# Optimization experiments

Hardware: AMD Instinct MI355X
Metric: run time of the kernel (lower is better)

Reference implementation:

```python
import jax, jax.numpy as jnp
import numpy as np
from jax import lax

B_SZ, D_SPEC, P, NC, MLP_D = 4096, 30, 9, 64, 64
L = P * P + 1  # 82 tokens (81 spiral + cls)


def _spiral_idx(patch=P):
    # Replicates Scan.forward's hardcoded assignments_map: center pixel, then
    # concentric rings (top row, right col, bottom row, left col), each of length 2r.
    cen = patch // 2
    rows, cols = [cen], [cen]
    for r in range(1, cen + 1):
        rows += [cen - r] * (2 * r); cols += list(range(cen - r + 1, cen + r + 1))
        rows += list(range(cen - r + 1, cen + r + 1)); cols += [cen + r] * (2 * r)
        rows += [cen + r] * (2 * r); cols += list(range(cen - r, cen + r))
        rows += list(range(cen - r, cen + r)); cols += [cen - r] * (2 * r)
    return np.asarray(rows), np.asarray(cols)

_ROWS, _COLS = _spiral_idx()


def _ln(x, g, b, eps=1e-5):
    m = x.mean(-1, keepdims=True)
    v = ((x - m) ** 2).mean(-1, keepdims=True)
    return (x - m) * lax.rsqrt(v + eps) * g + b


def _bn(x, g, b, m, v, nspatial, eps=1e-5):
    sh = (1, -1) + (1,) * nspatial
    return (x - m.reshape(sh)) * lax.rsqrt(v.reshape(sh) + eps) * g.reshape(sh) + b.reshape(sh)


def setup_inputs():
    key = jax.random.key(0)
    ks = iter(jax.random.split(key, 40))
    def rn(shape, s=0.1):
        return s * jax.random.normal(next(ks), shape, jnp.float32)
    return {
        "input_data": jax.random.normal(next(ks), (B_SZ, 1, D_SPEC, P, P), jnp.float32),
        "w3": rn((8, 1, 3, 3, 3)), "b3": rn((8,)),
        "g3": 1.0 + rn((8,)), "be3": rn((8,)), "m3": jnp.zeros((8,)), "v3": jnp.ones((8,)),
        "w2c": rn((NC, 8 * D_SPEC, 3, 3)), "b2c": rn((NC,)),
        "g2": 1.0 + rn((NC,)), "be2": rn((NC,)), "m2": jnp.zeros((NC,)), "v2": jnp.ones((NC,)),
        "pos_emb": rn((1, L, NC)), "cls_tok": rn((1, 1, NC)),
        "ln1_g": jnp.ones((NC,)), "ln1_b": jnp.zeros((NC,)),
        "Wb": rn((NC, NC)), "bb": rn((NC,)),
        "Wc": rn((NC, NC)), "bc": rn((NC,)),
        "Wd": rn((NC, NC)), "bd": rn((NC,)),
        "delta_p": rn((1, L, NC)), "A_p": rn((L, NC)),
        "Wst": rn((NC, NC)), "bst": rn((NC,)), "bias_st": rn((1, 1, NC)),
        "ln2_g": jnp.ones((NC,)), "ln2_b": jnp.zeros((NC,)),
        "Wm1": rn((NC, MLP_D)), "bm1": rn((MLP_D,)),
        "Wm2": rn((MLP_D, NC)), "bm2": rn((NC,)),
    }


def _forward(input_data, w3, b3, g3, be3, m3, v3, w2c, b2c, g2, be2, m2, v2,
             pos_emb, cls_tok, ln1_g, ln1_b, Wb, bb, Wc, bc, Wd, bd,
             delta_p, A_p, Wst, bst, bias_st, ln2_g, ln2_b, Wm1, bm1, Wm2, bm2):
    b = input_data.shape[0]
    # conv3d (SAME, k=3) + BN(eval) + ReLU
    h = lax.conv_general_dilated(input_data, w3, (1, 1, 1), [(1, 1)] * 3,
                                 dimension_numbers=("NCDHW", "OIDHW", "NCDHW"))
    h = jax.nn.relu(_bn(h + b3[None, :, None, None, None], g3, be3, m3, v3, 3))
    h = h.reshape(b, 8 * D_SPEC, P, P)  # 'b c h w y -> b (c h) w y'
    # conv2d (SAME, k=3) + BN(eval) + ReLU
    h = lax.conv_general_dilated(h, w2c, (1, 1), [(1, 1)] * 2,
                                 dimension_numbers=("NCHW", "OIHW", "NCHW"))
    h = jax.nn.relu(_bn(h + b2c[None, :, None, None], g2, be2, m2, v2, 2))
    # spiral scan gather: [B,C,H,W] -> [B,81,C]
    seq = jnp.transpose(h, (0, 2, 3, 1))[:, _ROWS, _COLS, :]
    tok = jnp.concatenate([jnp.broadcast_to(cls_tok, (b, 1, NC)), seq], axis=1) + pos_emb
    # (emb dropout = identity in eval)
    # --- Residual(LayerNormalize(S6_noC)) ---
    xn = _ln(tok, ln1_g, ln1_b)
    z = jax.nn.sigmoid(xn)
    B0 = xn @ Wb + bb
    C_ = xn @ Wc + bc
    sq = jnp.mean(xn, axis=1, keepdims=True)              # SToken squeeze [B,1,D]
    sq = jax.nn.sigmoid(jax.nn.relu(sq @ Wst + bst))
    T_ = (sq + bias_st) * xn                              # [B,L,D]
    delta = jax.nn.sigmoid(xn @ Wd + bd + delta_p)
    A_ = delta * A_p[None]                                # [B,L,D]
    Bx = delta * B0 * xn                                  # B_ * x fused
    def step(s, inp):
        a, bx, c, t = inp
        s = a * s + bx
        return s, c * s + t
    ins = (jnp.moveaxis(A_, 1, 0), jnp.moveaxis(Bx, 1, 0),
           jnp.moveaxis(C_, 1, 0), jnp.moveaxis(T_, 1, 0))  # [L,B,D]
    _, out = lax.scan(step, jnp.zeros((b, NC), xn.dtype), ins)
    tok = tok + jnp.moveaxis(out, 0, 1) * z               # residual
    # AdaptiveAvgPool1d(1) over seq + squeeze -> [B, D]
    pooled = tok.mean(axis=1)
    # --- Residual(LayerNormalize(MLP_Block)) (dropout = identity) ---
    yn = _ln(pooled, ln2_g, ln2_b)
    mlp = jax.nn.gelu(yn @ Wm1 + bm1, approximate=False) @ Wm2 + bm2
    return pooled + mlp


def reference(input_data, w3, b3, g3, be3, m3, v3, w2c, b2c, g2, be2, m2, v2,
              pos_emb, cls_tok, ln1_g, ln1_b, Wb, bb, Wc, bc, Wd, bd,
              delta_p, A_p, Wst, bst, bias_st, ln2_g, ln2_b, Wm1, bm1, Wm2, bm2):
    return _forward(input_data, w3, b3, g3, be3, m3, v3, w2c, b2c, g2, be2, m2, v2,
                    pos_emb, cls_tok, ln1_g, ln1_b, Wb, bb, Wc, bc, Wd, bd,
                    delta_p, A_p, Wst, bst, bias_st, ln2_g, ln2_b, Wm1, bm1, Wm2, bm2)
```

## Files before the change

### kernel.cpp

```cpp
#include <hip/hip_runtime.h>

typedef unsigned short u16;
typedef __attribute__((ext_vector_type(8))) short bf16x8;
typedef __attribute__((ext_vector_type(4))) float f32x4;
typedef __attribute__((ext_vector_type(4))) int i32x4;

#define DEV __device__ __forceinline__

DEV u16 f2bf(float f){
  unsigned u = __float_as_uint(f);
  u += 0x7fffu + ((u >> 16) & 1u);
  return (u16)(u >> 16);
}
DEV float bf2f(u16 h){ return __uint_as_float(((unsigned)h) << 16); }

DEV int spiral_t(int pix){
  int px = pix / 9, py = pix % 9;
  int dr = px - 4, dc = py - 4;
  int ar = dr < 0 ? -dr : dr, ac = dc < 0 ? -dc : dc;
  int r = ar > ac ? ar : ac;
  if (r == 0) return 0;
  int start = 1 + 4*r*(r-1);
  if (dr == -r && dc >= -r+1) return start + dc + r - 1;
  if (dc == r)  return start + 2*r + dr + r - 1;
  if (dr == r)  return start + 4*r + dc + r;
  return start + 6*r + dr + r;
}

__global__ __launch_bounds__(256) void k_wt(const float* __restrict__ w2c,
                                            const float* __restrict__ g2,
                                            const float* __restrict__ v2,
                                            u16* __restrict__ Wt2){
  int idx = blockIdx.x*256 + threadIdx.x;
  if (idx >= 72*64*32) return;
  int kk = idx & 31;
  int o  = (idx >> 5) & 63;
  int tile = idx >> 11;
  int dxy = tile >> 3;
  int chunk = tile & 7;
  int ch = chunk*32 + kk;
  float v = 0.f;
  if (ch < 240){
    float s2 = g2[o] * rsqrtf(v2[o] + 1e-5f);
    v = w2c[(o*240 + ch)*9 + dxy] * s2;
  }
  Wt2[idx] = f2bf(v);
}

__global__ __launch_bounds__(256) void k_conv3d(const float* __restrict__ x,
    const float* __restrict__ w3, const float* __restrict__ b3,
    const float* __restrict__ g3, const float* __restrict__ be3,
    const float* __restrict__ m3, const float* __restrict__ v3,
    u16* __restrict__ h1){
  __shared__ float tile[3872];
  __shared__ float wle[216];
  __shared__ float sc[8], sh[8];
  int b = blockIdx.x, tid = threadIdx.x;
  for (int i = tid; i < 3872; i += 256) tile[i] = 0.f;
  if (tid < 216) wle[tid] = w3[tid];
  if (tid < 8){
    float s = g3[tid]*rsqrtf(v3[tid]+1e-5f);
    sc[tid] = s;
    sh[tid] = (b3[tid]-m3[tid])*s + be3[tid];
  }
  __syncthreads();
  const float* xin = x + b*2430;
  for (int i = tid; i < 2430; i += 256){
    int dd = i / 81, rem = i % 81;
    int px = rem / 9, py = rem % 9;
    tile[(dd+1)*121 + (px+1)*11 + (py+1)] = xin[i];
  }
  __syncthreads();
  u16* hb = h1 + (size_t)b*19440;
  for (int p = tid; p < 2430; p += 256){
    int pix = p / 30, dd = p % 30;
    int px = pix / 9, py = pix % 9;
    const float* tp = tile + dd*121 + px*11 + py;
    float v[27];
    #pragma unroll
    for (int kd=0;kd<3;kd++)
      #pragma unroll
      for (int kx=0;kx<3;kx++)
        #pragma unroll
        for (int ky=0;ky<3;ky++)
          v[(kd*3+kx)*3+ky] = tp[kd*121 + kx*11 + ky];
    u16* hp = hb + pix*240 + dd;
    #pragma unroll
    for (int co=0;co<8;co++){
      float acc = 0.f;
      const float* wp = wle + co*27;
      #pragma unroll
      for (int q=0;q<27;q++) acc = fmaf(v[q], wp[q], acc);
      hp[co*30] = f2bf(fmaxf(acc*sc[co] + sh[co], 0.f));
    }
  }
}

__global__ __launch_bounds__(256, 2) void k_conv2d(const u16* __restrict__ h1,
    const u16* __restrict__ Wt2,
    const float* __restrict__ b2c, const float* __restrict__ g2,
    const float* __restrict__ be2, const float* __restrict__ m2,
    const float* __restrict__ v2,
    const float* __restrict__ pos_emb, const float* __restrict__ cls_tok,
    const float* __restrict__ ln1_g, const float* __restrict__ ln1_b,
    const float* __restrict__ Wst, const float* __restrict__ bst,
    const float* __restrict__ bias_st,
    u16* __restrict__ xn, float* __restrict__ tsum, float* __restrict__ sqs){
  __shared__ __align__(16) char smem[80848];
  const int ZROW = 80352;
  int tid = threadIdx.x;
  int wv = tid >> 6, ln = tid & 63;
  int lq = ln >> 4, lr = ln & 15;
  int img0 = blockIdx.x*2;
  size_t grow0 = (size_t)img0*81;

  int bln = lr*32 + lq*8;

#define LOADB(TAP, C, B)                                                        \
    { const u16* Bt_ = Wt2 + (TAP)*16384 + bln;                                 \
      _Pragma("unroll")                                                         \
      for (int kk=0;kk<2;kk++)                                                  \
        _Pragma("unroll")                                                       \
        for (int j=0;j<4;j++)                                                   \
          B[kk][j] = *(const bf16x8*)(Bt_ + ((C)*2+kk)*2048 + j*512); }

  bf16x8 bB0[2][4], bB1[2][4], bB2[2][4];
  LOADB(0, 0, bB0);
  LOADB(0, 1, bB1);
  LOADB(0, 2, bB2);

  for (int r = tid; r < 162; r += 256)
    *(i32x4*)(smem + r*496 + 480) = (i32x4){0,0,0,0};
  if (tid < 31) *(i32x4*)(smem + ZROW + tid*16) = (i32x4){0,0,0,0};
  {
    const u16* src = h1 + grow0*240;
    for (int idx = tid; idx < 162*30; idx += 256){
      int r = idx / 30, c = idx % 30;
      *(i32x4*)(smem + r*496 + c*16) = *(const i32x4*)(src + idx*8);
    }
  }
  __syncthreads();

  f32x4 acc[3][4];
  #pragma unroll
  for (int i=0;i<3;i++)
    #pragma unroll
    for (int j=0;j<4;j++) acc[i][j] = (f32x4){0.f,0.f,0.f,0.f};

#define CALCADDR(TAP, A0, A1, A13)                                              \
  { int dx = (TAP)/3 - 1, dy = (TAP)%3 - 1;                                     \
    _Pragma("unroll")                                                           \
    for (int rt=0;rt<3;rt++){                                                   \
      int row = (wv*3+rt)*16 + lr;                                              \
      int pix = row % 81;                                                       \
      int px = pix/9, py = pix%9;                                               \
      int px2 = px + dx, py2 = py + dy;                                         \
      bool valid = (row < 162) && ((unsigned)px2 < 9u) && ((unsigned)py2 < 9u); \
      int nrow = (row - pix) + px2*9 + py2;                                     \
      int base = valid ? nrow*496 : ZROW;                                       \
      A0[rt]  = base + lq*16;                                                   \
      A1[rt]  = base + 64 + lq*16;                                              \
      A13[rt] = (lq == 3) ? ZROW : (A1[rt] + 384);                              \
    } }

#define LOADA(C, SA0, SA1, SA13, A0, A1)                                        \
    { _Pragma("unroll")                                                         \
      for (int rt=0;rt<3;rt++){                                                 \
        A0[rt] = *(const bf16x8*)(smem + SA0[rt] + (C)*128);                    \
        A1[rt] = *(const bf16x8*)(smem + ((C)==3 ? SA13[rt]                     \
                                                 : SA1[rt] + (C)*128)); } }

#define DOMFMA(B, A0, A1)                                                       \
    { __builtin_amdgcn_s_setprio(1);                                            \
      _Pragma("unroll")                                                         \
      for (int rt=0;rt<3;rt++)                                                  \
        _Pragma("unroll")                                                       \
        for (int j=0;j<4;j++)                                                   \
          acc[rt][j] = __builtin_amdgcn_mfma_f32_16x16x32_bf16(A0[rt], B[0][j], acc[rt][j], 0, 0, 0); \
      _Pragma("unroll")                                                         \
      for (int rt=0;rt<3;rt++)                                                  \
        _Pragma("unroll")                                                       \
        for (int j=0;j<4;j++)                                                   \
          acc[rt][j] = __builtin_amdgcn_mfma_f32_16x16x32_bf16(A1[rt], B[1][j], acc[rt][j], 0, 0, 0); \
      __builtin_amdgcn_s_setprio(0); }

#define TAPBODY(TAPV, BA, BB, BC)                                               \
  { int ntap_ = (TAPV) < 8 ? (TAPV)+1 : 8;                                      \
    DOMFMA(BA, aAX0, aAX1);                                                     \
    LOADB((TAPV), 3, BA); LOADA(2, aC0, aC1, aC13, aAX0, aAX1);                 \
    DOMFMA(BB, aAY0, aAY1);                                                     \
    LOADB(ntap_, 0, BB); CALCADDR(ntap_, aN0, aN1, aN13);                       \
    LOADA(3, aC0, aC1, aC13, aAY0, aAY1);                                       \
    DOMFMA(BC, aAX0, aAX1);                                                     \
    LOADB(ntap_, 1, BC); LOADA(0, aN0, aN1, aN13, aAX0, aAX1);                  \
    DOMFMA(BA, aAY0, aAY1);                                                     \
    LOADB(ntap_, 2, BA); LOADA(1, aN0, aN1, aN13, aAY0, aAY1);                  \
    _Pragma("unroll")                                                           \
    for (int rt=0;rt<3;rt++){ aC0[rt]=aN0[rt]; aC1[rt]=aN1[rt]; aC13[rt]=aN13[rt]; } }

  int aC0[3], aC1[3], aC13[3];
  int aN0[3], aN1[3], aN13[3];
  bf16x8 aAX0[3], aAX1[3], aAY0[3], aAY1[3];

  CALCADDR(0, aC0, aC1, aC13);
  LOADA(0, aC0, aC1, aC13, aAX0, aAX1);
  LOADA(1, aC0, aC1, aC13, aAY0, aAY1);

  for (int t3 = 0; t3 < 9; t3 += 3){
    TAPBODY(t3+0, bB0, bB1, bB2);
    TAPBODY(t3+1, bB1, bB2, bB0);
    TAPBODY(t3+2, bB2, bB0, bB1);
  }
#undef CALCADDR
#undef LOADB
#undef LOADA
#undef DOMFMA
#undef TAPBODY

  __syncthreads();

  float t2c[4], lg[4], lb[4];
  #pragma unroll
  for (int j=0;j<4;j++){
    int col = j*16 + lr;
    float s2 = g2[col]*rsqrtf(v2[col]+1e-5f);
    t2c[j] = (b2c[col]-m2[col])*s2 + be2[col];
    lg[j] = ln1_g[col]; lb[j] = ln1_b[col];
  }

  float st0[4]={0,0,0,0}, st1[4]={0,0,0,0};
  float sx0[4]={0,0,0,0}, sx1[4]={0,0,0,0};

  #pragma unroll
  for (int rt=0;rt<3;rt++){
    #pragma unroll
    for (int e=0;e<4;e++){
      int row = (wv*3+rt)*16 + lq*4 + e;
      if (row < 162){
        int im = (row >= 81);
        int pix = row - im*81;
        int tsp = spiral_t(pix);
        const float* pe = pos_emb + (1+tsp)*64;
        float y[4], m1 = 0.f, m2v = 0.f;
        #pragma unroll
        for (int j=0;j<4;j++){
          y[j] = fmaxf(acc[rt][j][e] + t2c[j], 0.f) + pe[j*16+lr];
          m1 += y[j]; m2v = fmaf(y[j], y[j], m2v);
        }
        #pragma unroll
        for (int off=1; off<16; off<<=1){
          m1  += __shfl_xor(m1,  off, 64);
          m2v += __shfl_xor(m2v, off, 64);
        }
        float mean = m1*(1.f/64.f);
        float var  = m2v*(1.f/64.f) - mean*mean;
        float rs = rsqrtf(var + 1e-5f);
        u16* dst = xn + ((size_t)(img0+im)*82 + 1 + tsp)*64;
        #pragma unroll
        for (int j=0;j<4;j++){
          float xnv = (y[j]-mean)*rs*lg[j] + lb[j];
          dst[j*16+lr] = f2bf(xnv);
          if (im == 0){ st0[j] += y[j]; sx0[j] += xnv; }
          else        { st1[j] += y[j]; sx1[j] += xnv; }
        }
      }
    }
  }

  #pragma unroll
  for (int j=0;j<4;j++){
    st0[j] += __shfl_xor(st0[j],16,64); st0[j] += __shfl_xor(st0[j],32,64);
    st1[j] += __shfl_xor(st1[j],16,64); st1[j] += __shfl_xor(st1[j],32,64);
    sx0[j] += __shfl_xor(sx0[j],16,64); sx0[j] += __shfl_xor(sx0[j],32,64);
    sx1[j] += __shfl_xor(sx1[j],16,64); sx1[j] += __shfl_xor(sx1[j],32,64);
  }
  float* partT = (float*)smem;
  float* partX = (float*)(smem + 2048);
  float* xsumL = (float*)(smem + 4096);
  if (lq == 0){
    #pragma unroll
    for (int j=0;j<4;j++){
      partT[wv*128 +       j*16+lr] = st0[j];
      partT[wv*128 + 64  + j*16+lr] = st1[j];
      partX[wv*128 +       j*16+lr] = sx0[j];
      partX[wv*128 + 64  + j*16+lr] = sx1[j];
    }
  }
  __syncthreads();
  if (tid < 128){
    int im = tid >> 6, d = tid & 63;
    float tt = partT[im*64+d] + partT[128+im*64+d] + partT[256+im*64+d] + partT[384+im*64+d];
    float xx = partX[im*64+d] + partX[128+im*64+d] + partX[256+im*64+d] + partX[384+im*64+d];
    float clsv = cls_tok[d] + pos_emb[d];
    float c1v = clsv, c2v = clsv*clsv;
    #pragma unroll
    for (int off=1; off<64; off<<=1){ c1v += __shfl_xor(c1v, off, 64); c2v += __shfl_xor(c2v, off, 64); }
    float cm = c1v*(1.f/64.f), cv = c2v*(1.f/64.f) - cm*cm;
    float cxn = (clsv - cm)*rsqrtf(cv + 1e-5f)*ln1_g[d] + ln1_b[d];
    xn[((size_t)(img0+im)*82)*64 + d] = f2bf(cxn);
    tsum[(size_t)(img0+im)*64 + d] = tt + clsv;
    xsumL[im*64 + d] = (xx + cxn) * (1.f/82.f);
  }
  __syncthreads();
  {
    int im = tid >> 7, d2 = tid & 127;
    int d = d2 >> 1, half = d2 & 1;
    float a = 0.f;
    int k0 = half*32;
    #pragma unroll
    for (int k=0;k<32;k++) a = fmaf(xsumL[im*64 + k0+k], Wst[(k0+k)*64+d], a);
    a += __shfl_xor(a, 1, 64);
    if (half == 0){
      a += bst[d];
      a = fmaxf(a, 0.f);
      a = 1.f/(1.f + __expf(-a));
      sqs[(size_t)(img0+im)*64 + d] = a + bias_st[d];
    }
  }
}

__global__ __launch_bounds__(256, 2) void k_fuse(const u16* __restrict__ xn,
    const float* __restrict__ tsum, const float* __restrict__ sqs,
    const float* __restrict__ Wb, const float* __restrict__ Wc, const float* __restrict__ Wd,
    const float* __restrict__ bbv, const float* __restrict__ bcv, const float* __restrict__ bdv,
    const float* __restrict__ delta_p, const float* __restrict__ A_p,
    const float* __restrict__ ln2_g, const float* __restrict__ ln2_b,
    const float* __restrict__ Wm1, const float* __restrict__ bm1,
    const float* __restrict__ Wm2, const float* __restrict__ bm2,
    float* __restrict__ out){
  __shared__ __align__(16) char xnL[96*128];
  __shared__ u16 AxL[96][66], BxL[96][66], CxL[96][66];
  int tid = threadIdx.x;
  int wv = tid >> 6, ln = tid & 63;
  int lq = ln >> 4, lr = ln & 15;
  int b = blockIdx.x;

  bf16x8 bfr[3][2];
  {
    int cc = wv*16 + lr;
    const float* Ws[3] = {Wb, Wc, Wd};
    #pragma unroll
    for (int w=0;w<3;w++)
      #pragma unroll
      for (int kk=0;kk<2;kk++){
        int k0 = kk*32 + lq*8;
        bf16x8 f;
        #pragma unroll
        for (int e=0;e<8;e++) f[e] = (short)f2bf(Ws[w][(k0+e)*64 + cc]);
        bfr[w][kk] = f;
      }
  }

  {
    const u16* src = xn + (size_t)b*82*64;
    for (int idx = tid; idx < 656; idx += 256){
      int r = idx >> 3, c = idx & 7;
      *(i32x4*)(xnL + r*128 + ((c*16) ^ ((r&7)<<4))) = *(const i32x4*)(src + idx*8);
    }
    for (int idx = tid; idx < 112; idx += 256){
      int r = 82 + (idx >> 3), c = idx & 7;
      *(i32x4*)(xnL + r*128 + ((c*16) ^ ((r&7)<<4))) = (i32x4){0,0,0,0};
    }
  }
  __syncthreads();

  f32x4 acc[6][3];
  #pragma unroll
  for (int i=0;i<6;i++)
    #pragma unroll
    for (int w=0;w<3;w++) acc[i][w] = (f32x4){0.f,0.f,0.f,0.f};

  #pragma unroll
  for (int rt=0;rt<6;rt++){
    int row = rt*16 + lr;
    bf16x8 afr[2];
    #pragma unroll
    for (int kk=0;kk<2;kk++)
      afr[kk] = *(const bf16x8*)(xnL + row*128 + ((kk*64 + lq*16) ^ ((row&7)<<4)));
    #pragma unroll
    for (int kk=0;kk<2;kk++)
      #pragma unroll
      for (int w=0;w<3;w++)
        acc[rt][w] = __builtin_amdgcn_mfma_f32_16x16x32_bf16(afr[kk], bfr[w][kk], acc[rt][w], 0, 0, 0);
  }

  {
    int d = wv*16 + lr;
    float bB = bbv[d], bC = bcv[d], bD = bdv[d];
    #pragma unroll
    for (int rt=0;rt<6;rt++){
      #pragma unroll
      for (int e=0;e<4;e++){
        int t = rt*16 + lq*4 + e;
        if (t < 82){
          float B0 = acc[rt][0][e] + bB;
          float Cv = acc[rt][1][e] + bC;
          float Dr = acc[rt][2][e] + bD + delta_p[t*64+d];
          float D  = 1.f/(1.f + __expf(-Dr));
          float xv = bf2f(*(const u16*)(xnL + t*128 + ((d*2) ^ ((t&7)<<4))));
          AxL[t][d] = f2bf(D * A_p[t*64+d]);
          BxL[t][d] = f2bf(D * B0 * xv);
          CxL[t][d] = f2bf(Cv);
        }
      }
    }
  }
  __syncthreads();

  if (wv == 0){
    int d = ln;
    float sq = sqs[(size_t)b*64 + d];
    float s = 0.f, racc = 0.f;
    for (int t = 0; t < 82; t++){
      float a  = bf2f(AxL[t][d]);
      float bx = bf2f(BxL[t][d]);
      float c  = bf2f(CxL[t][d]);
      float xv = bf2f(*(const u16*)(xnL + t*128 + ((d*2) ^ ((t&7)<<4))));
      s = fmaf(a, s, bx);
      float o = fmaf(c, s, sq*xv);
      float z = 1.f/(1.f + __expf(-xv));
      racc = fmaf(o, z, racc);
    }
    float pooled = (tsum[(size_t)b*64 + d] + racc) * (1.f/82.f);
    float s1 = pooled, s2v = pooled*pooled;
    #pragma unroll
    for (int off=32; off>0; off>>=1){ s1 += __shfl_xor(s1, off, 64); s2v += __shfl_xor(s2v, off, 64); }
    float mean = s1*(1.f/64.f), var = s2v*(1.f/64.f) - mean*mean;
    float yn = (pooled - mean)*rsqrtf(var + 1e-5f)*ln2_g[d] + ln2_b[d];
    float a1 = bm1[d];
    for (int k=0;k<64;k++) a1 = fmaf(__shfl(yn, k, 64), Wm1[k*64+d], a1);
    float hg = 0.5f*a1*(1.f + erff(a1*0.70710678118654752f));
    float a2 = bm2[d];
    for (int k=0;k<64;k++) a2 = fmaf(__shfl(hg, k, 64), Wm2[k*64+d], a2);
    out[(size_t)b*64 + d] = pooled + a2;
  }
}

extern "C" void kernel_launch(void* const* d_in, const int* in_sizes, int n_in,
                              void* d_out, int out_size, void* d_ws, size_t ws_size,
                              hipStream_t stream){
  const float* x       = (const float*)d_in[0];
  const float* w3      = (const float*)d_in[1];
  const float* b3      = (const float*)d_in[2];
  const float* g3      = (const float*)d_in[3];
  const float* be3     = (const float*)d_in[4];
  const float* m3      = (const float*)d_in[5];
  const float* v3      = (const float*)d_in[6];
  const float* w2c     = (const float*)d_in[7];
  const float* b2c     = (const float*)d_in[8];
  const float* g2      = (const float*)d_in[9];
  const float* be2     = (const float*)d_in[10];
  const float* m2      = (const float*)d_in[11];
  const float* v2      = (const float*)d_in[12];
  const float* pos_emb = (const float*)d_in[13];
  const float* cls_tok = (const float*)d_in[14];
  const float* ln1_g   = (const float*)d_in[15];
  const float* ln1_b   = (const float*)d_in[16];
  const float* Wb      = (const float*)d_in[17];
  const float* bbv     = (const float*)d_in[18];
  const float* Wc      = (const float*)d_in[19];
  const float* bc      = (const float*)d_in[20];
  const float* Wd      = (const float*)d_in[21];
  const float* bd      = (const float*)d_in[22];
  const float* delta_p = (const float*)d_in[23];
  const float* A_p     = (const float*)d_in[24];
  const float* Wst     = (const float*)d_in[25];
  const float* bst     = (const float*)d_in[26];
  const float* bias_st = (const float*)d_in[27];
  const float* ln2_g   = (const float*)d_in[28];
  const float* ln2_b   = (const float*)d_in[29];
  const float* Wm1     = (const float*)d_in[30];
  const float* bm1     = (const float*)d_in[31];
  const float* Wm2     = (const float*)d_in[32];
  const float* bm2     = (const float*)d_in[33];

  char* ws = (char*)d_ws;
  u16*   h1   = (u16*)ws;
  u16*   Wt2  = (u16*)(ws + 159252480);
  u16*   xnb  = (u16*)(ws + 159571968);
  float* tsum = (float*)(ws + 202563584);
  float* sqs  = (float*)(ws + 203612160);

  k_wt    <<<576,  256, 0, stream>>>(w2c, g2, v2, Wt2);
  k_conv3d<<<4096, 256, 0, stream>>>(x, w3, b3, g3, be3, m3, v3, h1);
  k_conv2d<<<2048, 256, 0, stream>>>(h1, Wt2, b2c, g2, be2, m2, v2,
                                     pos_emb, cls_tok, ln1_g, ln1_b,
                                     Wst, bst, bias_st, xnb, tsum, sqs);
  k_fuse  <<<4096, 256, 0, stream>>>(xnb, tsum, sqs, Wb, Wc, Wd, bbv, bc, bd,
                                     delta_p, A_p, ln2_g, ln2_b,
                                     Wm1, bm1, Wm2, bm2, (float*)d_out);
}
```

Measured before the change: 383.4 us.

## Restructure conv3d so each thread sweeps depth with a rolling input window

The conv3d stage now assigns one thread per (pixel, output channel) instead of per (pixel, depth). Each thread keeps its 27 weights in registers and slides a three-slice window along depth, so every input slice is loaded from LDS once instead of up to three times. The 30 bf16 outputs are packed into 32-bit stores. This cuts LDS traffic and scalar 16-bit stores, but only 648 threads per block are active across three loop iterations and register pressure rises. The tile is padded with one more zero slice so the window's final loads stay in bounds.

```diff
diff --git a/kernel.cpp b/kernel.cpp
--- a/kernel.cpp
+++ b/kernel.cpp
@@ -1,6 +1,7 @@
 #include <hip/hip_runtime.h>
 
 typedef unsigned short u16;
+typedef unsigned int u32;
 typedef __attribute__((ext_vector_type(8))) short bf16x8;
 typedef __attribute__((ext_vector_type(4))) float f32x4;
 typedef __attribute__((ext_vector_type(4))) int i32x4;
@@ -52,11 +53,11 @@
     const float* __restrict__ g3, const float* __restrict__ be3,
     const float* __restrict__ m3, const float* __restrict__ v3,
     u16* __restrict__ h1){
-  __shared__ float tile[3872];
+  __shared__ float tile[3993];
   __shared__ float wle[216];
   __shared__ float sc[8], sh[8];
   int b = blockIdx.x, tid = threadIdx.x;
-  for (int i = tid; i < 3872; i += 256) tile[i] = 0.f;
+  for (int i = tid; i < 3993; i += 256) tile[i] = 0.f;
   if (tid < 216) wle[tid] = w3[tid];
   if (tid < 8){
     float s = g3[tid]*rsqrtf(v3[tid]+1e-5f);
@@ -72,27 +73,52 @@
   }
   __syncthreads();
   u16* hb = h1 + (size_t)b*19440;
-  for (int p = tid; p < 2430; p += 256){
-    int pix = p / 30, dd = p % 30;
+
+  for (int col = tid; col < 648; col += 256){
+    int pix = col >> 3, co = col & 7;
     int px = pix / 9, py = pix % 9;
-    const float* tp = tile + dd*121 + px*11 + py;
-    float v[27];
-    #pragma unroll
-    for (int kd=0;kd<3;kd++)
-      #pragma unroll
-      for (int kx=0;kx<3;kx++)
-        #pragma unroll
-        for (int ky=0;ky<3;ky++)
-          v[(kd*3+kx)*3+ky] = tp[kd*121 + kx*11 + ky];
-    u16* hp = hb + pix*240 + dd;
-    #pragma unroll
-    for (int co=0;co<8;co++){
-      float acc = 0.f;
-      const float* wp = wle + co*27;
-      #pragma unroll
-      for (int q=0;q<27;q++) acc = fmaf(v[q], wp[q], acc);
-      hp[co*30] = f2bf(fmaxf(acc*sc[co] + sh[co], 0.f));
-    }
+    const float* base = tile + px*11 + py;
+    float wp[27];
+    #pragma unroll
+    for (int q=0;q<27;q++) wp[q] = wle[co*27+q];
+    float scv = sc[co], shv = sh[co];
+
+    float s0[9], s1[9], s2[9];
+#define LSL(S, SL)                                                            \
+    { const float* tp2 = base + (SL)*121;                                     \
+      _Pragma("unroll")                                                       \
+      for (int kx=0;kx<3;kx++)                                                \
+        _Pragma("unroll")                                                     \
+        for (int ky=0;ky<3;ky++) S[kx*3+ky] = tp2[kx*11+ky]; }
+#define DOT3(A, SA, SB, SC)                                                   \
+    { A = 0.f;                                                                \
+      _Pragma("unroll")                                                       \
+      for (int q=0;q<9;q++) A = fmaf(SA[q], wp[q], A);                        \
+      _Pragma("unroll")                                                       \
+      for (int q=0;q<9;q++) A = fmaf(SB[q], wp[9+q], A);                      \
+      _Pragma("unroll")                                                       \
+      for (int q=0;q<9;q++) A = fmaf(SC[q], wp[18+q], A); }
+
+    LSL(s0, 0); LSL(s1, 1); LSL(s2, 2);
+    u16 outv[30];
+    #pragma unroll
+    for (int d3 = 0; d3 < 30; d3 += 3){
+      float a;
+      DOT3(a, s0, s1, s2);
+      outv[d3] = f2bf(fmaxf(fmaf(a, scv, shv), 0.f));
+      LSL(s0, d3+3);
+      DOT3(a, s1, s2, s0);
+      outv[d3+1] = f2bf(fmaxf(fmaf(a, scv, shv), 0.f));
+      LSL(s1, d3+4);
+      DOT3(a, s2, s0, s1);
+      outv[d3+2] = f2bf(fmaxf(fmaf(a, scv, shv), 0.f));
+      LSL(s2, d3+5);
+    }
+#undef LSL
+#undef DOT3
+    u32* dst = (u32*)(hb + pix*240 + co*30);
+    #pragma unroll
+    for (int q=0;q<15;q++) dst[q] = ((u32)outv[2*q+1] << 16) | (u32)outv[2*q];
   }
 }
 
```

Result: faster. 364.6 us (-4.9%).
